# Kernel tuning notes

Hardware: AMD Instinct MI355X
Metric: run time of the kernel (lower is better)

Reference implementation:

```python
import jax, jax.numpy as jnp
import numpy as np

CIR_LENGTH = 64
SYM_BLK = 64
NUM_BLK = 64
H = 2 * CIR_LENGTH * SYM_BLK  # 8192, hidden size = col_num * group_size
W_SCALE = 0.01  # keep tanh out of saturation


def setup_inputs() -> dict:
    key = jax.random.key(0)
    k_x, k_ih, k_hh, k_b = jax.random.split(key, 4)
    x = jax.random.normal(k_x, (NUM_BLK, H), dtype=jnp.float32)
    W_ih = jax.random.normal(k_ih, (H, H), dtype=jnp.float32) * W_SCALE
    W_hh = jax.random.normal(k_hh, (H, H), dtype=jnp.float32) * W_SCALE
    b = jax.random.normal(k_b, (H,), dtype=jnp.float32) * W_SCALE
    return {"x": x, "W_ih": W_ih, "W_hh": W_hh, "b": b}


def reference(x, W_ih, W_hh, b):
    # Shared-weight Elman RNN over NUM_BLK blocks (the torch ModuleList holds
    # NUM copies of the SAME template module, so weights are tied).
    h0 = jnp.zeros((H,), dtype=x.dtype)

    def step(h, x_t):
        h_new = jnp.tanh(x_t @ W_ih.T + h @ W_hh.T + b)
        return h_new, h_new

    _, hs = jax.lax.scan(step, h0, x)  # hs: (NUM_BLK, H)
    # est_channel: each step's hidden reshaped to (SYM_BLK, 2*CIR_LENGTH) rows
    return hs.reshape(NUM_BLK * SYM_BLK, 2 * CIR_LENGTH)
```

## Files before the change

### kernel.cpp

```cpp
#include <hip/hip_runtime.h>
#include <cmath>
#include <type_traits>


#define HDIM 8192
#define NSTEP 64
#define GRID_P 256
#define BLK_P 512
#define ROWS_B 32
#define R_W 4
#define NCH 16
#define NCH_REG 12
#define NCH_LDS 4
#define LDS_BYTES (16384 + 131072)

typedef _Float16 f16;
typedef _Float16 f16x2 __attribute__((ext_vector_type(2)));
typedef _Float16 f16x4 __attribute__((ext_vector_type(4)));
typedef _Float16 f16x8 __attribute__((ext_vector_type(8)));
typedef __fp16 fp16x2_raw __attribute__((ext_vector_type(2)));
typedef float f32x4 __attribute__((ext_vector_type(4)));

#if defined(__has_builtin)
#if __has_builtin(__builtin_amdgcn_fdot2)
#define HAS_FDOT2 1
#endif
#endif

__device__ __forceinline__ f16x2 pkrtz(float a, float b) {
  fp16x2_raw r = __builtin_amdgcn_cvt_pkrtz(a, b);
  return __builtin_bit_cast(f16x2, r);
}

__device__ __forceinline__ float dot8(f16x8 a, f16x8 b, float c) {
#ifdef HAS_FDOT2
  f16x2 a0 = {a[0], a[1]}, b0 = {b[0], b[1]};
  f16x2 a1 = {a[2], a[3]}, b1 = {b[2], b[3]};
  f16x2 a2 = {a[4], a[5]}, b2 = {b[4], b[5]};
  f16x2 a3 = {a[6], a[7]}, b3 = {b[6], b[7]};
  c = __builtin_amdgcn_fdot2(a0, b0, c, false);
  c = __builtin_amdgcn_fdot2(a1, b1, c, false);
  c = __builtin_amdgcn_fdot2(a2, b2, c, false);
  c = __builtin_amdgcn_fdot2(a3, b3, c, false);
  return c;
#else
  for (int i = 0; i < 8; i++) c += (float)a[i] * (float)b[i];
  return c;
#endif
}

__device__ __forceinline__ f16x8 cvt8(f32x4 a0, f32x4 a1) {
  f16x2 p0 = pkrtz(a0[0], a0[1]), p1 = pkrtz(a0[2], a0[3]);
  f16x2 p2 = pkrtz(a1[0], a1[1]), p3 = pkrtz(a1[2], a1[3]);
  return (f16x8){p0[0], p0[1], p1[0], p1[1], p2[0], p2[1], p3[0], p3[1]};
}

__global__ void cvt_f16_kernel(const float* __restrict__ src,
                               f16* __restrict__ dst, int n4) {
  int idx = blockIdx.x * blockDim.x + threadIdx.x;
  int stride = gridDim.x * blockDim.x;
  for (int i = idx; i < n4; i += stride) {
    f32x4 v = ((const f32x4*)src)[i];
    f16x4 h;
    h[0] = (f16)v[0]; h[1] = (f16)v[1]; h[2] = (f16)v[2]; h[3] = (f16)v[3];
    ((f16x4*)dst)[i] = h;
  }
}

template <bool XF16>
__global__ __launch_bounds__(256) void gemm_u_kernel(
    const float* __restrict__ x, const f16* __restrict__ x16,
    const float* __restrict__ Wih, const float* __restrict__ b,
    float* __restrict__ out) {
  const int wave = threadIdx.x >> 6;
  const int lane = threadIdx.x & 63;
  const int r = lane & 15, q = lane >> 4;
  const int n0 = blockIdx.x * 16;
  const int m0 = wave * 16;
  const float* wrow = Wih + (size_t)(n0 + r) * HDIM;
  f32x4 acc = {0.f, 0.f, 0.f, 0.f};
#pragma unroll 2
  for (int k0 = 0; k0 < HDIM; k0 += 32) {
    const int kb = k0 + q * 8;
    f16x8 fa;
    if constexpr (XF16) {
      fa = *(const f16x8*)(x16 + (size_t)(m0 + r) * HDIM + kb);
    } else {
      f32x4 a0 = *(const f32x4*)(x + (size_t)(m0 + r) * HDIM + kb);
      f32x4 a1 = *(const f32x4*)(x + (size_t)(m0 + r) * HDIM + kb + 4);
      fa = cvt8(a0, a1);
    }
    f32x4 b0 = *(const f32x4*)(wrow + kb);
    f32x4 b1 = *(const f32x4*)(wrow + kb + 4);
    f16x8 fb = cvt8(b0, b1);
    acc = __builtin_amdgcn_mfma_f32_16x16x32_f16(fa, fb, acc, 0, 0, 0);
  }
  const float bv = b[n0 + r];
#pragma unroll
  for (int i = 0; i < 4; i++) {
    out[(size_t)(m0 + q * 4 + i) * HDIM + n0 + r] = acc[i] + bv;
  }
}

__device__ __forceinline__ void gridbar(unsigned* bar, unsigned& my_gen) {
  __syncthreads();
  if (threadIdx.x == 0) {
    __threadfence();
    const unsigned target = my_gen + 1;
    const unsigned g = blockIdx.x & 7u;
    unsigned old = __hip_atomic_fetch_add(&bar[g * 64], 1u, __ATOMIC_ACQ_REL,
                                          __HIP_MEMORY_SCOPE_AGENT);
    if (old == 31u) {
      unsigned o2 = __hip_atomic_fetch_add(&bar[576], 1u, __ATOMIC_ACQ_REL,
                                           __HIP_MEMORY_SCOPE_AGENT);
      if (o2 == 7u) {
        for (int gg = 0; gg < 8; gg++)
          __hip_atomic_store(&bar[gg * 64], 0u, __ATOMIC_RELAXED,
                             __HIP_MEMORY_SCOPE_AGENT);
        __hip_atomic_store(&bar[576], 0u, __ATOMIC_RELAXED,
                           __HIP_MEMORY_SCOPE_AGENT);
        __hip_atomic_fetch_add(&bar[640], 1u, __ATOMIC_RELEASE,
                               __HIP_MEMORY_SCOPE_AGENT);
      }
    }
    while (__hip_atomic_load(&bar[640], __ATOMIC_ACQUIRE,
                             __HIP_MEMORY_SCOPE_AGENT) < target)
      __builtin_amdgcn_s_sleep(2);
  }
  my_gen++;
  __syncthreads();
}

extern __shared__ char smem_dyn[];
__global__ __launch_bounds__(BLK_P, 2) void persist_kernel(
    const float* __restrict__ Whh, float* __restrict__ out,
    f16* __restrict__ hbuf, unsigned* __restrict__ bar) {
  f16* h_lds = (f16*)smem_dyn;
  f16* w_lds = (f16*)(smem_dyn + 16384);
  const int tid = threadIdx.x;
  const int wave = tid >> 6, lane = tid & 63;
  const int j0 = blockIdx.x * ROWS_B;
  const int jb = j0 + wave * R_W;

  f16x8 wreg[R_W][NCH_REG];
#pragma unroll
  for (int r = 0; r < R_W; r++) {
    const float* wrow = Whh + (size_t)(jb + r) * HDIM;
#pragma unroll
    for (int c = 0; c < NCH; c++) {
      const int k = c * 512 + lane * 8;
      f32x4 a0 = *(const f32x4*)(wrow + k);
      f32x4 a1 = *(const f32x4*)(wrow + k + 4);
      f16x8 w8 = cvt8(a0, a1);
      if (c < NCH_REG) {
        wreg[r][c] = w8;
      } else {
        const int row_l = wave * R_W + r;
        *(f16x8*)(w_lds + ((size_t)(row_l * NCH_LDS + (c - NCH_REG)) * 64 + lane) * 8) = w8;
      }
    }
  }

  unsigned my_gen = 0;

  if (tid < ROWS_B) {
    const int j = j0 + tid;
    float v = tanhf(out[j]);
    out[j] = v;
    hbuf[j] = (f16)v;
  }
  gridbar(bar, my_gen);

  for (int t = 1; t < NSTEP; t++) {
    const f16* hprev = hbuf + ((t - 1) & 1) * HDIM;
#pragma unroll
    for (int i = 0; i < HDIM / 8 / BLK_P; i++) {
      const int idx = i * BLK_P + tid;
      ((f16x8*)h_lds)[idx] = ((const f16x8*)hprev)[idx];
    }
    __syncthreads();

    float u[R_W];
    if (lane == 0) {
#pragma unroll
      for (int r = 0; r < R_W; r++) u[r] = out[(size_t)t * HDIM + jb + r];
    }

    float acc[R_W] = {0.f, 0.f, 0.f, 0.f};
#pragma unroll
    for (int c = 0; c < NCH_REG; c++) {
      f16x8 hx = *(const f16x8*)(h_lds + c * 512 + lane * 8);
#pragma unroll
      for (int r = 0; r < R_W; r++) acc[r] = dot8(wreg[r][c], hx, acc[r]);
    }
#pragma unroll
    for (int cc = 0; cc < NCH_LDS; cc++) {
      f16x8 hx = *(const f16x8*)(h_lds + (NCH_REG + cc) * 512 + lane * 8);
#pragma unroll
      for (int r = 0; r < R_W; r++) {
        const int row_l = wave * R_W + r;
        f16x8 wl = *(const f16x8*)(w_lds + ((size_t)(row_l * NCH_LDS + cc) * 64 + lane) * 8);
        acc[r] = dot8(wl, hx, acc[r]);
      }
    }

#pragma unroll
    for (int off = 32; off >= 1; off >>= 1) {
      acc[0] += __shfl_down(acc[0], off, 64);
      acc[1] += __shfl_down(acc[1], off, 64);
      acc[2] += __shfl_down(acc[2], off, 64);
      acc[3] += __shfl_down(acc[3], off, 64);
    }
    if (lane == 0) {
      f16* hcur = hbuf + (t & 1) * HDIM;
#pragma unroll
      for (int r = 0; r < R_W; r++) {
        float v = tanhf(u[r] + acc[r]);
        out[(size_t)t * HDIM + jb + r] = v;
        hcur[jb + r] = (f16)v;
      }
    }
    if (t < NSTEP - 1) gridbar(bar, my_gen);
  }
}

__global__ void step0_kernel(float* __restrict__ out) {
  int i = blockIdx.x * blockDim.x + threadIdx.x;
  out[i] = tanhf(out[i]);
}

__global__ __launch_bounds__(1024) void step_kernel_f32(
    const float* __restrict__ W, float* __restrict__ out, int t) {
  __shared__ float hs[HDIM];
  const float* hprev = out + (size_t)(t - 1) * HDIM;
  {
    const f32x4* hp4 = (const f32x4*)hprev;
#pragma unroll
    for (int i = 0; i < HDIM / 4 / 1024; i++) {
      const int idx = i * 1024 + threadIdx.x;
      *(f32x4*)&hs[idx * 4] = hp4[idx];
    }
  }
  __syncthreads();
  const int wave = threadIdx.x >> 6, lane = threadIdx.x & 63;
  const int j = blockIdx.x * 16 + wave;
  const float* wrow = W + (size_t)j * HDIM;
  float acc = 0.f;
#pragma unroll 4
  for (int it = 0; it < 16; it++) {
    const int kb = it * 512 + lane * 8;
    f32x4 w0 = *(const f32x4*)(wrow + kb);
    f32x4 w1 = *(const f32x4*)(wrow + kb + 4);
    const float* hp = &hs[kb];
    acc += w0[0] * hp[0] + w0[1] * hp[1] + w0[2] * hp[2] + w0[3] * hp[3];
    acc += w1[0] * hp[4] + w1[1] * hp[5] + w1[2] * hp[6] + w1[3] * hp[7];
  }
#pragma unroll
  for (int off = 32; off >= 1; off >>= 1) acc += __shfl_down(acc, off, 64);
  if (lane == 0) {
    const float u = out[(size_t)t * HDIM + j];
    out[(size_t)t * HDIM + j] = tanhf(u + acc);
  }
}

extern "C" void kernel_launch(void* const* d_in, const int* in_sizes, int n_in,
                              void* d_out, int out_size, void* d_ws,
                              size_t ws_size, hipStream_t stream) {
  const float* x = (const float*)d_in[0];
  const float* Wih = (const float*)d_in[1];
  const float* Whh = (const float*)d_in[2];
  const float* b = (const float*)d_in[3];
  float* out = (float*)d_out;

  const size_t need = 65536 + (size_t)NSTEP * HDIM * sizeof(f16);
  if (ws_size >= need) {
    unsigned* bar = (unsigned*)d_ws;
    f16* hbuf = (f16*)((char*)d_ws + 4096);
    f16* x16 = (f16*)((char*)d_ws + 65536);
    hipMemsetAsync(d_ws, 0, 4096, stream);
    cvt_f16_kernel<<<64, 256, 0, stream>>>(x, x16, NSTEP * HDIM / 4);
    gemm_u_kernel<true><<<HDIM / 16, 256, 0, stream>>>(x, x16, Wih, b, out);
    hipFuncSetAttribute((const void*)persist_kernel,
                        hipFuncAttributeMaxDynamicSharedMemorySize, LDS_BYTES);
    persist_kernel<<<GRID_P, BLK_P, LDS_BYTES, stream>>>(Whh, out, hbuf, bar);
  } else {
    gemm_u_kernel<false><<<HDIM / 16, 256, 0, stream>>>(x, nullptr, Wih, b, out);
    step0_kernel<<<HDIM / 256, 256, 0, stream>>>(out);
    for (int t = 1; t < NSTEP; t++)
      step_kernel_f32<<<HDIM / 16, 1024, 0, stream>>>(Whh, out, t);
  }
}
```

Before: 2.218 ms.

## Replace grid barrier with per-step flag arrays and stream part of W_hh from global

The hierarchical atomic grid barrier is replaced by per-step, per-block ready flags: each block publishes a flag after writing its slice of h, and wave 0 of every block polls all 256 flags for the previous step before loading h. The h buffer now keeps every step instead of ping-ponging between two, so no barrier reset is needed. Register-resident W_hh chunks drop from 12 to 8 to cut register pressure, and the 4 freed chunks are kept as f16 in a global workspace and reloaded every step (likely from L2). The GEMM unroll also grows from 2 to 8. The trade-off is extra global/L2 weight traffic each step and the polling of 256 flags per block per step.

```diff
diff --git a/kernel.cpp b/kernel.cpp
--- a/kernel.cpp
+++ b/kernel.cpp
@@ -10,8 +10,9 @@
 #define ROWS_B 32
 #define R_W 4
 #define NCH 16
-#define NCH_REG 12
+#define NCH_REG 8
 #define NCH_LDS 4
+#define NCH_STR 4
 #define LDS_BYTES (16384 + 131072)
 
 typedef _Float16 f16;
@@ -79,7 +80,7 @@
   const int m0 = wave * 16;
   const float* wrow = Wih + (size_t)(n0 + r) * HDIM;
   f32x4 acc = {0.f, 0.f, 0.f, 0.f};
-#pragma unroll 2
+#pragma unroll 8
   for (int k0 = 0; k0 < HDIM; k0 += 32) {
     const int kb = k0 + q * 8;
     f16x8 fa;
@@ -102,45 +103,19 @@
   }
 }
 
-__device__ __forceinline__ void gridbar(unsigned* bar, unsigned& my_gen) {
-  __syncthreads();
-  if (threadIdx.x == 0) {
-    __threadfence();
-    const unsigned target = my_gen + 1;
-    const unsigned g = blockIdx.x & 7u;
-    unsigned old = __hip_atomic_fetch_add(&bar[g * 64], 1u, __ATOMIC_ACQ_REL,
-                                          __HIP_MEMORY_SCOPE_AGENT);
-    if (old == 31u) {
-      unsigned o2 = __hip_atomic_fetch_add(&bar[576], 1u, __ATOMIC_ACQ_REL,
-                                           __HIP_MEMORY_SCOPE_AGENT);
-      if (o2 == 7u) {
-        for (int gg = 0; gg < 8; gg++)
-          __hip_atomic_store(&bar[gg * 64], 0u, __ATOMIC_RELAXED,
-                             __HIP_MEMORY_SCOPE_AGENT);
-        __hip_atomic_store(&bar[576], 0u, __ATOMIC_RELAXED,
-                           __HIP_MEMORY_SCOPE_AGENT);
-        __hip_atomic_fetch_add(&bar[640], 1u, __ATOMIC_RELEASE,
-                               __HIP_MEMORY_SCOPE_AGENT);
-      }
-    }
-    while (__hip_atomic_load(&bar[640], __ATOMIC_ACQUIRE,
-                             __HIP_MEMORY_SCOPE_AGENT) < target)
-      __builtin_amdgcn_s_sleep(2);
-  }
-  my_gen++;
-  __syncthreads();
-}
-
 extern __shared__ char smem_dyn[];
-__global__ __launch_bounds__(BLK_P, 2) void persist_kernel(
-    const float* __restrict__ Whh, float* __restrict__ out,
-    f16* __restrict__ hbuf, unsigned* __restrict__ bar) {
+__global__ __launch_bounds__(BLK_P)
+__attribute__((amdgpu_waves_per_eu(2, 2)))
+void persist_kernel(const float* __restrict__ Whh, float* __restrict__ out,
+                    f16* __restrict__ hbuf, f16* __restrict__ wstream,
+                    unsigned* __restrict__ flags) {
   f16* h_lds = (f16*)smem_dyn;
   f16* w_lds = (f16*)(smem_dyn + 16384);
   const int tid = threadIdx.x;
   const int wave = tid >> 6, lane = tid & 63;
   const int j0 = blockIdx.x * ROWS_B;
   const int jb = j0 + wave * R_W;
+  f16* sptr = wstream + (size_t)(blockIdx.x * 8 + wave) * (R_W * NCH_STR * 512);
 
   f16x8 wreg[R_W][NCH_REG];
 #pragma unroll
@@ -154,14 +129,14 @@
       f16x8 w8 = cvt8(a0, a1);
       if (c < NCH_REG) {
         wreg[r][c] = w8;
-      } else {
+      } else if (c < NCH_REG + NCH_LDS) {
         const int row_l = wave * R_W + r;
         *(f16x8*)(w_lds + ((size_t)(row_l * NCH_LDS + (c - NCH_REG)) * 64 + lane) * 8) = w8;
+      } else {
+        *(f16x8*)(sptr + ((size_t)(r * NCH_STR + (c - NCH_REG - NCH_LDS)) * 64 + lane) * 8) = w8;
       }
     }
   }
-
-  unsigned my_gen = 0;
 
   if (tid < ROWS_B) {
     const int j = j0 + tid;
@@ -169,22 +144,48 @@
     out[j] = v;
     hbuf[j] = (f16)v;
   }
-  gridbar(bar, my_gen);
+  __syncthreads();
+  if (tid == 0) {
+    __threadfence();
+    __hip_atomic_store(&flags[blockIdx.x], 1u, __ATOMIC_RELEASE,
+                       __HIP_MEMORY_SCOPE_AGENT);
+  }
 
   for (int t = 1; t < NSTEP; t++) {
-    const f16* hprev = hbuf + ((t - 1) & 1) * HDIM;
+    float u[R_W];
+    if (lane == 0) {
+#pragma unroll
+      for (int r = 0; r < R_W; r++) u[r] = out[(size_t)t * HDIM + jb + r];
+    }
+    if (wave == 0) {
+      const unsigned* fb = flags + (size_t)(t - 1) * 256 + lane * 4;
+      bool ok;
+      do {
+        unsigned f0 = __hip_atomic_load(&fb[0], __ATOMIC_ACQUIRE, __HIP_MEMORY_SCOPE_AGENT);
+        unsigned f1 = __hip_atomic_load(&fb[1], __ATOMIC_ACQUIRE, __HIP_MEMORY_SCOPE_AGENT);
+        unsigned f2 = __hip_atomic_load(&fb[2], __ATOMIC_ACQUIRE, __HIP_MEMORY_SCOPE_AGENT);
+        unsigned f3 = __hip_atomic_load(&fb[3], __ATOMIC_ACQUIRE, __HIP_MEMORY_SCOPE_AGENT);
+        ok = (f0 & f1 & f2 & f3) != 0u;
+        if (!__all(ok)) __builtin_amdgcn_s_sleep(1);
+        else break;
+      } while (true);
+    }
+    __syncthreads();
+
+    const f16x8* hsrc8 = (const f16x8*)(hbuf + (size_t)(t - 1) * HDIM);
 #pragma unroll
     for (int i = 0; i < HDIM / 8 / BLK_P; i++) {
       const int idx = i * BLK_P + tid;
-      ((f16x8*)h_lds)[idx] = ((const f16x8*)hprev)[idx];
+      ((f16x8*)h_lds)[idx] = hsrc8[idx];
     }
     __syncthreads();
 
-    float u[R_W];
-    if (lane == 0) {
-#pragma unroll
-      for (int r = 0; r < R_W; r++) u[r] = out[(size_t)t * HDIM + jb + r];
-    }
+    f16x8 sw[R_W][NCH_STR];
+#pragma unroll
+    for (int r = 0; r < R_W; r++)
+#pragma unroll
+      for (int cc = 0; cc < NCH_STR; cc++)
+        sw[r][cc] = *(const f16x8*)(sptr + ((size_t)(r * NCH_STR + cc) * 64 + lane) * 8);
 
     float acc[R_W] = {0.f, 0.f, 0.f, 0.f};
 #pragma unroll
@@ -203,6 +204,12 @@
         acc[r] = dot8(wl, hx, acc[r]);
       }
     }
+#pragma unroll
+    for (int cc = 0; cc < NCH_STR; cc++) {
+      f16x8 hx = *(const f16x8*)(h_lds + (NCH_REG + NCH_LDS + cc) * 512 + lane * 8);
+#pragma unroll
+      for (int r = 0; r < R_W; r++) acc[r] = dot8(sw[r][cc], hx, acc[r]);
+    }
 
 #pragma unroll
     for (int off = 32; off >= 1; off >>= 1) {
@@ -212,7 +219,7 @@
       acc[3] += __shfl_down(acc[3], off, 64);
     }
     if (lane == 0) {
-      f16* hcur = hbuf + (t & 1) * HDIM;
+      f16* hcur = hbuf + (size_t)t * HDIM;
 #pragma unroll
       for (int r = 0; r < R_W; r++) {
         float v = tanhf(u[r] + acc[r]);
@@ -220,7 +227,12 @@
         hcur[jb + r] = (f16)v;
       }
     }
-    if (t < NSTEP - 1) gridbar(bar, my_gen);
+    __syncthreads();
+    if (t < NSTEP - 1 && tid == 0) {
+      __threadfence();
+      __hip_atomic_store(&flags[(size_t)t * 256 + blockIdx.x], 1u,
+                         __ATOMIC_RELEASE, __HIP_MEMORY_SCOPE_AGENT);
+    }
   }
 }
 
@@ -272,17 +284,24 @@
   const float* b = (const float*)d_in[3];
   float* out = (float*)d_out;
 
-  const size_t need = 65536 + (size_t)NSTEP * HDIM * sizeof(f16);
+  const size_t off_flags = 0;
+  const size_t off_hbuf = 65536;
+  const size_t off_x16 = 65536 + (1u << 20);
+  const size_t off_wstr = 65536 + (2u << 20);
+  const size_t need = off_wstr + (size_t)GRID_P * 8 * R_W * NCH_STR * 512 * sizeof(f16);
+
   if (ws_size >= need) {
-    unsigned* bar = (unsigned*)d_ws;
-    f16* hbuf = (f16*)((char*)d_ws + 4096);
-    f16* x16 = (f16*)((char*)d_ws + 65536);
-    hipMemsetAsync(d_ws, 0, 4096, stream);
+    unsigned* flags = (unsigned*)((char*)d_ws + off_flags);
+    f16* hbuf = (f16*)((char*)d_ws + off_hbuf);
+    f16* x16 = (f16*)((char*)d_ws + off_x16);
+    f16* wstream = (f16*)((char*)d_ws + off_wstr);
+    hipMemsetAsync(d_ws, 0, 65536, stream);
     cvt_f16_kernel<<<64, 256, 0, stream>>>(x, x16, NSTEP * HDIM / 4);
     gemm_u_kernel<true><<<HDIM / 16, 256, 0, stream>>>(x, x16, Wih, b, out);
     hipFuncSetAttribute((const void*)persist_kernel,
                         hipFuncAttributeMaxDynamicSharedMemorySize, LDS_BYTES);
-    persist_kernel<<<GRID_P, BLK_P, LDS_BYTES, stream>>>(Whh, out, hbuf, bar);
+    persist_kernel<<<GRID_P, BLK_P, LDS_BYTES, stream>>>(Whh, out, hbuf,
+                                                         wstream, flags);
   } else {
     gemm_u_kernel<false><<<HDIM / 16, 256, 0, stream>>>(x, nullptr, Wih, b, out);
     step0_kernel<<<HDIM / 256, 256, 0, stream>>>(out);
```

Measured after the change: 2.451 ms. 10.5% more time.
